# Optimization experiments

Measured on AMD Instinct MI355X. Metric: run time of the kernel, lower is better.

## Reference

```python
import jax, jax.numpy as jnp
import numpy as np
from jax import lax

D_MODEL = 1024
N_EXPERTS = 8
N_ACTIVE = 2
FFN_HIDDEN = int(D_MODEL * 2.0)


def setup_inputs() -> dict:
    key = jax.random.key(0)
    ks = jax.random.split(key, 7)
    B, T = 2, 2048
    s_in = 1.0 / np.sqrt(D_MODEL)
    s_h = 1.0 / np.sqrt(FFN_HIDDEN)
    return {
        "x": jax.random.normal(ks[0], (B, T, D_MODEL), dtype=jnp.float32),
        # router: torch Linear(d_model, n_experts, bias=False) weight [E, D]
        "router_w": jax.random.uniform(ks[1], (N_EXPERTS, D_MODEL), jnp.float32, -s_in, s_in),
        # stacked expert FFN params: w1 [E, H, D], b1 [E, H], w2 [E, D, H], b2 [E, D]
        "w1": jax.random.uniform(ks[2], (N_EXPERTS, FFN_HIDDEN, D_MODEL), jnp.float32, -s_in, s_in),
        "b1": jax.random.uniform(ks[3], (N_EXPERTS, FFN_HIDDEN), jnp.float32, -s_in, s_in),
        "w2": jax.random.uniform(ks[4], (N_EXPERTS, D_MODEL, FFN_HIDDEN), jnp.float32, -s_h, s_h),
        "b2": jax.random.uniform(ks[5], (N_EXPERTS, D_MODEL), jnp.float32, -s_h, s_h),
    }


def reference(x, router_w, w1, b1, w2, b2):
    B, T, D = x.shape
    N = B * T
    xf = x.reshape(N, D)

    logits = xf @ router_w.T                      # [N, E]
    probs = jax.nn.softmax(logits, axis=-1)       # [N, E]

    # --- aux load-balancing loss (f_i is non-differentiable, from indices) ---
    _, disp_idx = lax.top_k(logits, N_ACTIVE)     # [N, K]
    disp_mask = jax.nn.one_hot(disp_idx, N_EXPERTS, dtype=logits.dtype).sum(axis=1)  # [N, E]
    f_i = disp_mask.sum(axis=0) / (N * N_ACTIVE)  # [E]
    P_i = probs.mean(axis=0)                      # [E]
    aux_loss = N_EXPERTS * jnp.sum(f_i * P_i)

    # --- top-k combine weights, renormalized ---
    topk_w, topk_idx = lax.top_k(probs, N_ACTIVE)                 # [N, K]
    topk_w = topk_w / topk_w.sum(axis=-1, keepdims=True)
    # scatter top-k weights into dense [N, E] combine matrix (zeros elsewhere)
    combine_w = (jax.nn.one_hot(topk_idx, N_EXPERTS, dtype=xf.dtype) * topk_w[..., None]).sum(axis=1)

    # --- expert FFNs, weighted combine (loop over small fixed expert set) ---
    out = jnp.zeros_like(xf)
    for e in range(N_EXPERTS):
        h = jax.nn.silu(xf @ w1[e].T + b1[e])     # [N, H]
        y = h @ w2[e].T + b2[e]                   # [N, D]
        out = out + combine_w[:, e:e + 1] * y

    return out.reshape(B, T, D), aux_loss
```

## Files before the change

### kernel.cpp

```cpp
#include <hip/hip_runtime.h>
#include <cstdint>
#include <cstddef>

#define D_MODEL 1024
#define N_EXPERTS 8
#define FFN_H 2048
#define N_TOK 4096
#define CAP 2048

typedef float f32x4 __attribute__((ext_vector_type(4)));
typedef __bf16 bf16x8 __attribute__((ext_vector_type(8)));

static constexpr size_t XB_OFF   = 0;
static constexpr size_t W1B_OFF  = XB_OFF  + (size_t)N_TOK * D_MODEL * 2;
static constexpr size_t W2B_OFF  = W1B_OFF + (size_t)N_EXPERTS * FFN_H * D_MODEL * 2;
static constexpr size_t HBUF_OFF = W2B_OFF + (size_t)N_EXPERTS * D_MODEL * FFN_H * 2;
static constexpr size_t YBUF_OFF = HBUF_OFF + (size_t)N_EXPERTS * CAP * FFN_H * 2;
static constexpr size_t CNT_OFF  = YBUF_OFF + (size_t)N_EXPERTS * CAP * D_MODEL * 2;
static constexpr size_t PSUM_OFF = CNT_OFF + 32;
static constexpr size_t TOK_OFF  = PSUM_OFF + 32;
static constexpr size_t TIX_OFF  = TOK_OFF + (size_t)N_EXPERTS * CAP * 4;
static constexpr size_t TIW_OFF  = TIX_OFF + (size_t)N_TOK * 8;

__device__ __forceinline__ void async_ld16(const void* g, void* l) {
    __builtin_amdgcn_global_load_lds(
        (const __attribute__((address_space(1))) unsigned int*)g,
        (__attribute__((address_space(3))) unsigned int*)l, 16, 0, 0);
}

__global__ __launch_bounds__(256) void prep_kernel(const float* __restrict__ x,
                                                   const float* __restrict__ rw,
                                                   const float* __restrict__ w1,
                                                   const float* __restrict__ w2,
                                                   __bf16* __restrict__ xb,
                                                   __bf16* __restrict__ w1b,
                                                   __bf16* __restrict__ w2b,
                                                   int* __restrict__ counts,
                                                   float* __restrict__ psum,
                                                   int* __restrict__ tok_list,
                                                   int2* __restrict__ tinfo_idx,
                                                   float2* __restrict__ tinfo_w) {
    __shared__ float rws[N_EXPERTS * D_MODEL];
    __shared__ int s_e0[64], s_e1[64], s_r0[64], s_r1[64];
    __shared__ float s_w0[64], s_w1[64];
    __shared__ int hist[8], base[8];
    __shared__ float pacc[8];

    int tid = threadIdx.x;
    int b = blockIdx.x;
    if (b >= 64) {
        int c = b - 64;
        const float* src; __bf16* dst; size_t bb;
        if (c < 2048)       { src = x;  dst = xb;  bb = (size_t)c * 2048; }
        else if (c < 10240) { src = w1; dst = w1b; bb = (size_t)(c - 2048) * 2048; }
        else                { src = w2; dst = w2b; bb = (size_t)(c - 10240) * 2048; }
        size_t i = bb + (size_t)tid * 8;
        float4 a = *reinterpret_cast<const float4*>(src + i);
        float4 d = *reinterpret_cast<const float4*>(src + i + 4);
        bf16x8 r;
        r[0] = (__bf16)a.x; r[1] = (__bf16)a.y; r[2] = (__bf16)a.z; r[3] = (__bf16)a.w;
        r[4] = (__bf16)d.x; r[5] = (__bf16)d.y; r[6] = (__bf16)d.z; r[7] = (__bf16)d.w;
        *reinterpret_cast<bf16x8*>(dst + i) = r;
        return;
    }

    for (int i = tid * 4; i < N_EXPERTS * D_MODEL; i += 256 * 4)
        *reinterpret_cast<float4*>(&rws[i]) = *reinterpret_cast<const float4*>(&rw[i]);
    if (tid < 8) { hist[tid] = 0; pacc[tid] = 0.f; }
    __syncthreads();

    int wave = tid >> 6, lane = tid & 63;
    float psacc[8] = {};
    for (int it = 0; it < 16; ++it) {
        int li = wave * 16 + it;
        int t = b * 64 + li;
        const float* xr = x + (size_t)t * D_MODEL;
        float acc[8] = {};
#pragma unroll
        for (int i = 0; i < D_MODEL / 64; ++i) {
            float xv = xr[lane + 64 * i];
#pragma unroll
            for (int e = 0; e < 8; ++e) acc[e] += xv * rws[e * D_MODEL + lane + 64 * i];
        }
        float logit[8];
#pragma unroll
        for (int e = 0; e < 8; ++e) {
            float v = acc[e];
            for (int off = 32; off; off >>= 1) v += __shfl_xor(v, off);
            logit[e] = v;
        }
        float mx = logit[0];
#pragma unroll
        for (int e = 1; e < 8; ++e) mx = fmaxf(mx, logit[e]);
        float p[8], s = 0.f;
#pragma unroll
        for (int e = 0; e < 8; ++e) { p[e] = expf(logit[e] - mx); s += p[e]; }
        float inv = 1.f / s;
#pragma unroll
        for (int e = 0; e < 8; ++e) { p[e] *= inv; psacc[e] += p[e]; }
        int e0 = 0; float p0 = p[0];
#pragma unroll
        for (int e = 1; e < 8; ++e) if (p[e] > p0) { p0 = p[e]; e0 = e; }
        int e1 = -1; float p1 = -1.f;
#pragma unroll
        for (int e = 0; e < 8; ++e) if (e != e0 && p[e] > p1) { p1 = p[e]; e1 = e; }
        float invw = 1.f / (p0 + p1);
        if (lane == 0) {
            s_e0[li] = e0; s_e1[li] = e1;
            s_w0[li] = p0 * invw; s_w1[li] = p1 * invw;
        }
    }
    if (lane == 0)
#pragma unroll
        for (int e = 0; e < 8; ++e) atomicAdd(&pacc[e], psacc[e]);
    __syncthreads();

    if (tid < 64) {
        s_r0[tid] = atomicAdd(&hist[s_e0[tid]], 1);
        s_r1[tid] = atomicAdd(&hist[s_e1[tid]], 1);
    }
    __syncthreads();
    if (tid < 8) {
        base[tid] = atomicAdd(&counts[tid], hist[tid]);
        atomicAdd(&psum[tid], pacc[tid]);
    }
    __syncthreads();
    if (tid < 64) {
        int t = b * 64 + tid;
        int e0 = s_e0[tid], e1 = s_e1[tid];
        int q0 = min(base[e0] + s_r0[tid], CAP - 1);
        int q1 = min(base[e1] + s_r1[tid], CAP - 1);
        tok_list[e0 * CAP + q0] = t;
        tok_list[e1 * CAP + q1] = t;
        tinfo_idx[t] = make_int2(e0 * CAP + q0, e1 * CAP + q1);
        tinfo_w[t] = make_float2(s_w0[tid], s_w1[tid]);
    }
}

template <int KDIM, bool PASS2>
__global__ __launch_bounds__(256, 2) void ffn_kernel(const __bf16* __restrict__ A_base,
                                                     const __bf16* __restrict__ B_base,
                                                     const float* __restrict__ bias,
                                                     const int* __restrict__ counts,
                                                     const int* __restrict__ tok_list,
                                                     __bf16* __restrict__ Out_base) {
    constexpr int BROWS = PASS2 ? D_MODEL : FFN_H;
    constexpr int NT = BROWS / 128;
    constexpr int NSTEP = KDIM / 64;
    int bid = blockIdx.x;
    int e = bid & 7;
    int r = bid >> 3;
    int n0 = (r % NT) * 128;
    int m0 = (r / NT) * 128;
    int cnt = min(counts[e], CAP);
    if (m0 >= cnt) return;

    __shared__ char smem[65536];

    int tid = threadIdx.x;
    int* s_tok = (int*)smem;
    if (!PASS2 && tid < 128) {
        int slot = min(m0 + tid, cnt - 1);
        s_tok[tid] = tok_list[e * CAP + slot];
    }
    __syncthreads();

    int colk = ((tid & 3) ^ ((tid >> 3) & 3)) * 8;
    const __bf16 *a_src0, *a_src1;
    if (PASS2) {
        int s0 = min(m0 + (tid >> 2), cnt - 1);
        int s1 = min(m0 + 64 + (tid >> 2), cnt - 1);
        a_src0 = A_base + ((size_t)e * CAP + s0) * KDIM + colk;
        a_src1 = A_base + ((size_t)e * CAP + s1) * KDIM + colk;
    } else {
        a_src0 = A_base + (size_t)s_tok[tid >> 2] * KDIM + colk;
        a_src1 = A_base + (size_t)s_tok[64 + (tid >> 2)] * KDIM + colk;
    }
    const __bf16* b_src0 = B_base + ((size_t)e * BROWS + n0 + (tid >> 2)) * KDIM + colk;
    const __bf16* b_src1 = b_src0 + (size_t)64 * KDIM;
    __syncthreads();

    int wv = tid >> 6, lane = tid & 63;
    int wm = wv >> 1, wn = wv & 1;
    int lm = lane & 15, q = lane >> 4;
    int rsw = ((q ^ ((lm >> 1) & 3)) * 8);
    int a_base = (wm * 64 + lm) * 32 + rsw;
    int b_base = (wn * 64 + lm) * 32 + rsw;

    char* wofs_a = smem + (tid >> 6) * 1024;
    char* wofs_b = smem + 32768 + (tid >> 6) * 1024;

    f32x4 acc[4][4] = {};

    {
        char* la = wofs_a; char* lb = wofs_b;
        async_ld16(a_src0,      la);        async_ld16(a_src1,      la + 4096);
        async_ld16(a_src0 + 32, la + 8192); async_ld16(a_src1 + 32, la + 8192 + 4096);
        async_ld16(b_src0,      lb);        async_ld16(b_src1,      lb + 4096);
        async_ld16(b_src0 + 32, lb + 8192); async_ld16(b_src1 + 32, lb + 8192 + 4096);
    }
    __syncthreads();

    int cur = 0;
    for (int t = 0; t < NSTEP; ++t) {
        if (t + 1 < NSTEP) {
            int k0 = (t + 1) * 64;
            char* la = wofs_a + ((cur ^ 1) * 16384);
            char* lb = wofs_b + ((cur ^ 1) * 16384);
            async_ld16(a_src0 + k0,      la);        async_ld16(a_src1 + k0,      la + 4096);
            async_ld16(a_src0 + k0 + 32, la + 8192); async_ld16(a_src1 + k0 + 32, la + 8192 + 4096);
            async_ld16(b_src0 + k0,      lb);        async_ld16(b_src1 + k0,      lb + 4096);
            async_ld16(b_src0 + k0 + 32, lb + 8192); async_ld16(b_src1 + k0 + 32, lb + 8192 + 4096);
        }
#pragma unroll
        for (int kk = 0; kk < 2; ++kk) {
            const __bf16* pa = (const __bf16*)(smem + (cur * 2 + kk) * 8192);
            const __bf16* pb = (const __bf16*)(smem + 32768 + (cur * 2 + kk) * 8192);
            bf16x8 af[4], bfg[4];
#pragma unroll
            for (int f = 0; f < 4; ++f) {
                af[f]  = *reinterpret_cast<const bf16x8*>(&pa[a_base + f * 16 * 32]);
                bfg[f] = *reinterpret_cast<const bf16x8*>(&pb[b_base + f * 16 * 32]);
            }
#pragma unroll
            for (int fm = 0; fm < 4; ++fm)
#pragma unroll
                for (int fn = 0; fn < 4; ++fn)
                    acc[fm][fn] = __builtin_amdgcn_mfma_f32_16x16x32_bf16(af[fm], bfg[fn], acc[fm][fn], 0, 0, 0);
        }
        __syncthreads();
        cur ^= 1;
    }

    __bf16* ep = (__bf16*)(smem) + wv * (64 * 72);
#pragma unroll
    for (int fn = 0; fn < 4; ++fn) {
        int n = n0 + wn * 64 + fn * 16 + lm;
        float bv = bias[e * BROWS + n];
#pragma unroll
        for (int fm = 0; fm < 4; ++fm)
#pragma unroll
            for (int i = 0; i < 4; ++i) {
                float v = acc[fm][fn][i] + bv;
                if (!PASS2) v = v / (1.f + __expf(-v));
                ep[(fm * 16 + q * 4 + i) * 72 + fn * 16 + lm] = (__bf16)v;
            }
    }
    __syncthreads();
    int rr = lane >> 3, ccol = (lane & 7) * 8;
#pragma unroll
    for (int rep = 0; rep < 8; ++rep) {
        int rw = rep * 8 + rr;
        int slot = m0 + wm * 64 + rw;
        bf16x8 vv = *reinterpret_cast<const bf16x8*>(&ep[rw * 72 + ccol]);
        if (slot < cnt)
            *reinterpret_cast<bf16x8*>(
                &Out_base[((size_t)e * CAP + slot) * BROWS + n0 + wn * 64 + ccol]) = vv;
    }
}

__global__ __launch_bounds__(256) void combine_kernel(const __bf16* __restrict__ ybuf,
                                                      const int2* __restrict__ tinfo_idx,
                                                      const float2* __restrict__ tinfo_w,
                                                      const int* __restrict__ counts,
                                                      const float* __restrict__ psum,
                                                      float* __restrict__ out) {
    int tid = threadIdx.x;
    if (blockIdx.x == 0 && tid == 0) {
        float s = 0.f;
#pragma unroll
        for (int e = 0; e < 8; ++e)
            s += ((float)counts[e] / (float)(N_TOK * 2)) * (psum[e] / (float)N_TOK);
        out[(size_t)N_TOK * D_MODEL] = 8.f * s;
    }
    int t = blockIdx.x * 2 + (tid >> 7);
    int d0 = (tid & 127) * 8;
    int2 ix = tinfo_idx[t];
    float2 w = tinfo_w[t];
    bf16x8 ya = *reinterpret_cast<const bf16x8*>(ybuf + (size_t)ix.x * D_MODEL + d0);
    bf16x8 yb = *reinterpret_cast<const bf16x8*>(ybuf + (size_t)ix.y * D_MODEL + d0);
    float4 o0, o1;
    o0.x = w.x * (float)ya[0] + w.y * (float)yb[0];
    o0.y = w.x * (float)ya[1] + w.y * (float)yb[1];
    o0.z = w.x * (float)ya[2] + w.y * (float)yb[2];
    o0.w = w.x * (float)ya[3] + w.y * (float)yb[3];
    o1.x = w.x * (float)ya[4] + w.y * (float)yb[4];
    o1.y = w.x * (float)ya[5] + w.y * (float)yb[5];
    o1.z = w.x * (float)ya[6] + w.y * (float)yb[6];
    o1.w = w.x * (float)ya[7] + w.y * (float)yb[7];
    float* op = out + (size_t)t * D_MODEL + d0;
    *reinterpret_cast<float4*>(op) = o0;
    *reinterpret_cast<float4*>(op + 4) = o1;
}

extern "C" void kernel_launch(void* const* d_in, const int* in_sizes, int n_in,
                              void* d_out, int out_size, void* d_ws, size_t ws_size,
                              hipStream_t stream) {
    const float* x  = (const float*)d_in[0];
    const float* rw = (const float*)d_in[1];
    const float* w1 = (const float*)d_in[2];
    const float* b1 = (const float*)d_in[3];
    const float* w2 = (const float*)d_in[4];
    const float* b2 = (const float*)d_in[5];
    float* out = (float*)d_out;

    char* ws = (char*)d_ws;
    __bf16* xb     = (__bf16*)(ws + XB_OFF);
    __bf16* w1b    = (__bf16*)(ws + W1B_OFF);
    __bf16* w2b    = (__bf16*)(ws + W2B_OFF);
    __bf16* hbuf   = (__bf16*)(ws + HBUF_OFF);
    __bf16* ybuf   = (__bf16*)(ws + YBUF_OFF);
    int*    counts = (int*)(ws + CNT_OFF);
    float*  psum   = (float*)(ws + PSUM_OFF);
    int*    tok    = (int*)(ws + TOK_OFF);
    int2*   tix    = (int2*)(ws + TIX_OFF);
    float2* tiw    = (float2*)(ws + TIW_OFF);

    hipMemsetAsync(ws + CNT_OFF, 0, 64, stream);

    prep_kernel<<<64 + 18432, 256, 0, stream>>>(x, rw, w1, w2, xb, w1b, w2b,
                                                counts, psum, tok, tix, tiw);

    ffn_kernel<D_MODEL, false><<<8 * (FFN_H / 128) * (CAP / 128), 256, 0, stream>>>(
        xb, w1b, b1, counts, tok, hbuf);
    ffn_kernel<FFN_H, true><<<8 * (D_MODEL / 128) * (CAP / 128), 256, 0, stream>>>(
        hbuf, w2b, b2, counts, tok, ybuf);

    combine_kernel<<<N_TOK / 2, 256, 0, stream>>>(ybuf, tix, tiw, counts, psum, out);
}
```

Measured before the change: 293.5 us.

## Deepen FFN GEMM K-pipeline to 4-stage ring with fine-grained vmcnt waits

The FFN GEMM main loop is rebuilt from a double-buffered 64-wide K step into a 4-slot ring of 32-wide K slices, with three slices prefetched ahead. Each iteration uses partial s_waitcnt vmcnt counts plus a raw s_barrier instead of a full __syncthreads after compute. The aim is to hide global-to-LDS load latency behind the MFMA work. Bias loads are hoisted before the loop, and s_setprio is raised around the MFMA block. The tighter synchronisation relies on the vmcnt counts matching exactly and doubles the barrier count per unit of K.

```diff
diff --git a/kernel.cpp b/kernel.cpp
--- a/kernel.cpp
+++ b/kernel.cpp
@@ -27,6 +27,9 @@
         (const __attribute__((address_space(1))) unsigned int*)g,
         (__attribute__((address_space(3))) unsigned int*)l, 16, 0, 0);
 }
+
+#define VMWAIT(n) asm volatile("s_waitcnt vmcnt(" #n ")" ::: "memory")
+#define SBAR()    asm volatile("s_barrier" ::: "memory")
 
 __global__ __launch_bounds__(256) void prep_kernel(const float* __restrict__ x,
                                                    const float* __restrict__ rw,
@@ -146,7 +149,7 @@
                                                      __bf16* __restrict__ Out_base) {
     constexpr int BROWS = PASS2 ? D_MODEL : FFN_H;
     constexpr int NT = BROWS / 128;
-    constexpr int NSTEP = KDIM / 64;
+    constexpr int NSTEP = KDIM / 32;
     int bid = blockIdx.x;
     int e = bid & 7;
     int r = bid >> 3;
@@ -183,65 +186,71 @@
     int wv = tid >> 6, lane = tid & 63;
     int wm = wv >> 1, wn = wv & 1;
     int lm = lane & 15, q = lane >> 4;
-    int rsw = ((q ^ ((lm >> 1) & 3)) * 8);
+    int rsw = (q ^ ((lm >> 1) & 3)) * 8;
     int a_base = (wm * 64 + lm) * 32 + rsw;
     int b_base = (wn * 64 + lm) * 32 + rsw;
-
-    char* wofs_a = smem + (tid >> 6) * 1024;
-    char* wofs_b = smem + 32768 + (tid >> 6) * 1024;
+    int wofs = (tid >> 6) * 1024;
+
+    float bv[4];
+    {
+        int nb = e * BROWS + n0 + wn * 64 + lm;
+#pragma unroll
+        for (int fn = 0; fn < 4; ++fn) bv[fn] = bias[nb + fn * 16];
+    }
+    VMWAIT(0);
 
     f32x4 acc[4][4] = {};
 
-    {
-        char* la = wofs_a; char* lb = wofs_b;
-        async_ld16(a_src0,      la);        async_ld16(a_src1,      la + 4096);
-        async_ld16(a_src0 + 32, la + 8192); async_ld16(a_src1 + 32, la + 8192 + 4096);
-        async_ld16(b_src0,      lb);        async_ld16(b_src1,      lb + 4096);
-        async_ld16(b_src0 + 32, lb + 8192); async_ld16(b_src1 + 32, lb + 8192 + 4096);
-    }
-    __syncthreads();
-
-    int cur = 0;
-    for (int t = 0; t < NSTEP; ++t) {
-        if (t + 1 < NSTEP) {
-            int k0 = (t + 1) * 64;
-            char* la = wofs_a + ((cur ^ 1) * 16384);
-            char* lb = wofs_b + ((cur ^ 1) * 16384);
-            async_ld16(a_src0 + k0,      la);        async_ld16(a_src1 + k0,      la + 4096);
-            async_ld16(a_src0 + k0 + 32, la + 8192); async_ld16(a_src1 + k0 + 32, la + 8192 + 4096);
-            async_ld16(b_src0 + k0,      lb);        async_ld16(b_src1 + k0,      lb + 4096);
-            async_ld16(b_src0 + k0 + 32, lb + 8192); async_ld16(b_src1 + k0 + 32, lb + 8192 + 4096);
+    auto stage = [&](int t) {
+        int k0 = t * 32;
+        int b4 = (t & 3) * 8192;
+        char* la = smem + b4 + wofs;
+        char* lb = smem + 32768 + b4 + wofs;
+        async_ld16(a_src0 + k0, la);
+        async_ld16(a_src1 + k0, la + 4096);
+        async_ld16(b_src0 + k0, lb);
+        async_ld16(b_src1 + k0, lb + 4096);
+    };
+    auto compute = [&](int t) {
+        int b4 = (t & 3) * 8192;
+        const __bf16* pa = (const __bf16*)(smem + b4);
+        const __bf16* pb = (const __bf16*)(smem + 32768 + b4);
+        bf16x8 af[4], bfg[4];
+#pragma unroll
+        for (int f = 0; f < 4; ++f) {
+            af[f]  = *reinterpret_cast<const bf16x8*>(&pa[a_base + f * 512]);
+            bfg[f] = *reinterpret_cast<const bf16x8*>(&pb[b_base + f * 512]);
         }
-#pragma unroll
-        for (int kk = 0; kk < 2; ++kk) {
-            const __bf16* pa = (const __bf16*)(smem + (cur * 2 + kk) * 8192);
-            const __bf16* pb = (const __bf16*)(smem + 32768 + (cur * 2 + kk) * 8192);
-            bf16x8 af[4], bfg[4];
-#pragma unroll
-            for (int f = 0; f < 4; ++f) {
-                af[f]  = *reinterpret_cast<const bf16x8*>(&pa[a_base + f * 16 * 32]);
-                bfg[f] = *reinterpret_cast<const bf16x8*>(&pb[b_base + f * 16 * 32]);
-            }
-#pragma unroll
-            for (int fm = 0; fm < 4; ++fm)
-#pragma unroll
-                for (int fn = 0; fn < 4; ++fn)
-                    acc[fm][fn] = __builtin_amdgcn_mfma_f32_16x16x32_bf16(af[fm], bfg[fn], acc[fm][fn], 0, 0, 0);
-        }
-        __syncthreads();
-        cur ^= 1;
-    }
+        __builtin_amdgcn_s_setprio(1);
+#pragma unroll
+        for (int fm = 0; fm < 4; ++fm)
+#pragma unroll
+            for (int fn = 0; fn < 4; ++fn)
+                acc[fm][fn] = __builtin_amdgcn_mfma_f32_16x16x32_bf16(af[fm], bfg[fn], acc[fm][fn], 0, 0, 0);
+        __builtin_amdgcn_s_setprio(0);
+    };
+
+    stage(0); stage(1); stage(2);
+
+    for (int t = 0; t < NSTEP - 3; ++t) {
+        VMWAIT(8);
+        SBAR();
+        stage(t + 3);
+        compute(t);
+    }
+    VMWAIT(8); SBAR(); compute(NSTEP - 3);
+    VMWAIT(4); SBAR(); compute(NSTEP - 2);
+    VMWAIT(0); SBAR(); compute(NSTEP - 1);
+    __syncthreads();
 
     __bf16* ep = (__bf16*)(smem) + wv * (64 * 72);
 #pragma unroll
     for (int fn = 0; fn < 4; ++fn) {
-        int n = n0 + wn * 64 + fn * 16 + lm;
-        float bv = bias[e * BROWS + n];
 #pragma unroll
         for (int fm = 0; fm < 4; ++fm)
 #pragma unroll
             for (int i = 0; i < 4; ++i) {
-                float v = acc[fm][fn][i] + bv;
+                float v = acc[fm][fn][i] + bv[fn];
                 if (!PASS2) v = v / (1.f + __expf(-v));
                 ep[(fm * 16 + q * 4 + i) * 72 + fn * 16 + lm] = (__bf16)v;
             }
```

Result: no change. 294.1 us (+0.2%).
